# Kernel optimization log

Hardware: AMD Instinct MI355X
Metric: run time of the kernel (lower is better)

Reference implementation:

```python
import jax, jax.numpy as jnp
import numpy as np

N_STATE = 64
N_LAYERS = 4
D_MODEL = 512
D_OUT = 256
BATCH = 16
SEQLEN = 2048


def setup_inputs() -> dict:
    key = jax.random.key(0)
    ks = jax.random.split(key, 16)
    H, N, nl = D_MODEL, N_STATE, N_LAYERS
    inp = {}
    inp["x"] = jax.random.normal(ks[0], (BATCH, SEQLEN, D_MODEL), dtype=jnp.float32)
    # encoder / decoder dense
    inp["enc_w"] = jax.random.normal(ks[1], (D_MODEL, D_MODEL), jnp.float32) / np.sqrt(D_MODEL)
    inp["enc_b"] = jnp.zeros((D_MODEL,), jnp.float32)
    inp["dec_w"] = jax.random.normal(ks[2], (D_MODEL, D_OUT), jnp.float32) / np.sqrt(D_MODEL)
    inp["dec_b"] = jnp.zeros((D_OUT,), jnp.float32)
    # per-layer LayerNorm
    inp["ln_scale"] = jnp.ones((nl, D_MODEL), jnp.float32)
    inp["ln_bias"] = jnp.zeros((nl, D_MODEL), jnp.float32)
    # per-layer S4 DPLR params (stored as real/imag float pairs)
    inp["lambda_re"] = -0.5 * jnp.ones((nl, H, N), jnp.float32)
    inp["lambda_im"] = jnp.broadcast_to(np.pi * jnp.arange(N, dtype=jnp.float32), (nl, H, N))
    inp["p_re"] = jax.random.normal(ks[3], (nl, H, N), jnp.float32) * 0.5
    inp["p_im"] = jax.random.normal(ks[4], (nl, H, N), jnp.float32) * 0.5
    inp["b_re"] = jax.random.normal(ks[5], (nl, H, N), jnp.float32) * 0.5
    inp["b_im"] = jax.random.normal(ks[6], (nl, H, N), jnp.float32) * 0.5
    inp["c_re"] = jax.random.normal(ks[7], (nl, H, N), jnp.float32) * 0.5
    inp["c_im"] = jax.random.normal(ks[8], (nl, H, N), jnp.float32) * 0.5
    inp["log_step"] = jax.random.uniform(ks[9], (nl, H), jnp.float32, minval=np.log(1e-3), maxval=np.log(1e-1))
    inp["d_param"] = jnp.ones((nl, H), jnp.float32)
    # per-layer output Dense
    inp["out_w"] = jax.random.normal(ks[10], (nl, D_MODEL, D_MODEL), jnp.float32) / np.sqrt(D_MODEL)
    inp["out_b"] = jnp.zeros((nl, D_MODEL), jnp.float32)
    return inp


def _layer_norm(x, scale, bias, eps=1e-6):
    mu = jnp.mean(x, axis=-1, keepdims=True)
    var = jnp.mean(jnp.square(x - mu), axis=-1, keepdims=True)
    return (x - mu) * jax.lax.rsqrt(var + eps) * scale + bias


def _kernel_dplr(Lam, P, B, C, step, L):
    # Lam,P,B,C: [H,N] complex64; step: [H] float32 -> K: [H,L] float32
    theta = (2.0 * np.pi / L) * jnp.arange(L, dtype=jnp.float32)
    Omega = jnp.exp(-1j * theta)                        # [L] roots of unity
    g = (2.0 / step)[:, None] * ((1.0 - Omega) / (1.0 + Omega))[None, :]  # [H,L]
    c = 2.0 / (1.0 + Omega)                             # [L]
    r = 1.0 / (g[:, :, None] - Lam[:, None, :])         # [H,L,N] resolvent (Cauchy)
    Cc, Pc = jnp.conj(C), jnp.conj(P)
    k00 = jnp.einsum("hn,hln->hl", Cc * B, r)
    k01 = jnp.einsum("hn,hln->hl", Cc * P, r)
    k10 = jnp.einsum("hn,hln->hl", Pc * B, r)
    k11 = jnp.einsum("hn,hln->hl", Pc * P, r)
    at_roots = c[None, :] * (k00 - k01 * (1.0 / (1.0 + k11)) * k10)  # [H,L]
    return jnp.fft.ifft(at_roots, n=L, axis=-1).real


def _s4_apply(u, Lam, P, B, C, step, D):
    # u: [Bt,L,H]; causal FFT convolution with kernel K[h,:] per channel
    L = u.shape[1]
    K = _kernel_dplr(Lam, P, B, C, step, L)             # [H,L]
    ud = jnp.fft.rfft(u, n=2 * L, axis=1)               # [Bt,L+1,H]
    Kd = jnp.fft.rfft(K, n=2 * L, axis=-1)              # [H,L+1]
    y = jnp.fft.irfft(ud * Kd.T[None], n=2 * L, axis=1)[:, :L]
    return y + D[None, None, :] * u


def reference(x, enc_w, enc_b, ln_scale, ln_bias, lambda_re, lambda_im,
              p_re, p_im, b_re, b_im, c_re, c_im, log_step, d_param,
              out_w, out_b, dec_w, dec_b):
    h = x @ enc_w + enc_b
    n_layers = ln_scale.shape[0]
    for i in range(n_layers):
        skip = h
        z = _layer_norm(h, ln_scale[i], ln_bias[i])
        Lam = lambda_re[i] + 1j * lambda_im[i]
        P = p_re[i] + 1j * p_im[i]
        B = b_re[i] + 1j * b_im[i]
        C = c_re[i] + 1j * c_im[i]
        z = _s4_apply(z, Lam, P, B, C, jnp.exp(log_step[i]), d_param[i])
        z = jax.nn.gelu(z)
        z = z @ out_w[i] + out_b[i]
        h = skip + z  # dropout=0.0 -> identity
    logits = h @ dec_w + dec_b
    return jax.nn.log_softmax(logits, axis=-1)
```

## Files before the change

### kernel.cpp

```cpp
#include <hip/hip_runtime.h>
#include <hip/hip_bf16.h>

#define NLAY 4
#define DH   512
#define NST  64
#define NB   16
#define SL   2048
#define NDO  256
#define BL   (NB*SL)
#define KDIM 512
#define TWOPI 6.283185307179586476925287

typedef unsigned short u16;
typedef __attribute__((ext_vector_type(8))) short  short8v;
typedef __attribute__((ext_vector_type(8))) unsigned short ushort8v;
typedef __attribute__((ext_vector_type(4))) float  f32x4;

#define RCPF(x) __builtin_amdgcn_rcpf(x)

__device__ __forceinline__ float bf2f(u16 v){
  union { unsigned u; float f; } x; x.u = ((unsigned)v) << 16; return x.f;
}
__device__ __forceinline__ u16 f2bf(float f){
  union { float f; unsigned u; } x; x.f = f;
  unsigned u = x.u;
  unsigned r = u + 0x7fffu + ((u >> 16) & 1u);
  return (u16)(r >> 16);
}
__device__ __forceinline__ void cmulw(float& xr, float& xi, float wr, float wi){
  float tr = xr*wr - xi*wi;
  xi = fmaf(xr, wi, xi*wr);
  xr = tr;
}
__device__ __forceinline__ float gelu_fast(float v){
  const float c0 = 0.7978845608028654f;
  float u = c0 * fmaf(0.044715f, v*v*v, v);
  return v * RCPF(1.0f + __expf(-2.0f * u));
}

template<int SGN>
__device__ __forceinline__ void dft4w(float& r0, float& i0, float& r1, float& i1,
                                      float& r2, float& i2, float& r3, float& i3){
  const float t0r = r0 + r2, t0i = i0 + i2;
  const float t1r = r0 - r2, t1i = i0 - i2;
  const float t2r = r1 + r3, t2i = i1 + i3;
  const float t3r = r1 - r3, t3i = i1 - i3;
  r0 = t0r + t2r; i0 = t0i + t2i;
  r2 = t0r - t2r; i2 = t0i - t2i;
  if (SGN < 0){ r1 = t1r + t3i; i1 = t1i - t3r; r3 = t1r - t3i; i3 = t1i + t3r; }
  else        { r1 = t1r - t3i; i1 = t1i + t3r; r3 = t1r + t3i; i3 = t1i - t3r; }
}

template<int SGN>
__device__ __forceinline__ void dft16(float* re, float* im){
#pragma unroll
  for (int b = 0; b < 4; b++)
    dft4w<SGN>(re[b], im[b], re[4+b], im[4+b], re[8+b], im[8+b], re[12+b], im[12+b]);
  const float C1 = 0.92387953251128675613f, S1_ = 0.38268343236508977172f;
  const float C2 = 0.70710678118654752440f;
  const float sg = (SGN < 0) ? -1.f : 1.f;
  cmulw(re[5],  im[5],   C1,  sg*S1_);
  cmulw(re[9],  im[9],   C2,  sg*C2);
  cmulw(re[13], im[13],  S1_, sg*C1);
  cmulw(re[6],  im[6],   C2,  sg*C2);
  cmulw(re[10], im[10],  0.f, sg*1.f);
  cmulw(re[14], im[14], -C2,  sg*C2);
  cmulw(re[7],  im[7],   S1_, sg*C1);
  cmulw(re[11], im[11], -C2,  sg*C2);
  cmulw(re[15], im[15], -C1,  sg*(-S1_));
#pragma unroll
  for (int c = 0; c < 4; c++)
    dft4w<SGN>(re[4*c], im[4*c], re[4*c+1], im[4*c+1], re[4*c+2], im[4*c+2], re[4*c+3], im[4*c+3]);
  float tr_, ti_;
#define SWP(A,B) tr_=re[A]; re[A]=re[B]; re[B]=tr_; ti_=im[A]; im[A]=im[B]; im[B]=ti_;
  SWP(1,4) SWP(2,8) SWP(3,12) SWP(6,9) SWP(7,13) SWP(11,14)
#undef SWP
}

__device__ __forceinline__ int cxpad(int i){ return i + (i >> 4) + ((i >> 8) << 1); }
#define CXSZ 4384

__device__ __forceinline__ void fwd4096(float* re, float* im, float2* cx, int t){
  dft16<-1>(re, im);
  const float a0 = -(float)(TWOPI/4096.0) * (float)t;
#pragma unroll
  for (int k = 0; k < 16; k++){
    if (k){ float sn = __sinf(a0*(float)k), cs = __cosf(a0*(float)k); cmulw(re[k], im[k], cs, sn); }
    cx[cxpad(t + 256*k)] = make_float2(re[k], im[k]);
  }
  __syncthreads();
  const int k1 = t >> 4, m2 = t & 15;
  const int b2 = k1*256 + m2;
#pragma unroll
  for (int j = 0; j < 16; j++){ float2 v = cx[cxpad(b2 + 16*j)]; re[j] = v.x; im[j] = v.y; }
  dft16<-1>(re, im);
  const float b0 = -(float)(TWOPI/256.0) * (float)m2;
#pragma unroll
  for (int k = 0; k < 16; k++){
    if (k){ float sn = __sinf(b0*(float)k), cs = __cosf(b0*(float)k); cmulw(re[k], im[k], cs, sn); }
    cx[cxpad(b2 + 16*k)] = make_float2(re[k], im[k]);
  }
  __syncthreads();
#pragma unroll
  for (int j = 0; j < 16; j++){ float2 v = cx[cxpad(16*t + j)]; re[j] = v.x; im[j] = v.y; }
  dft16<-1>(re, im);
}

__device__ __forceinline__ void inv4096(float* re, float* im, float2* cx, int t){
  dft16<1>(re, im);
#pragma unroll
  for (int j = 0; j < 16; j++) cx[cxpad(16*t + j)] = make_float2(re[j], im[j]);
  __syncthreads();
  const int k1 = t >> 4, m2 = t & 15;
  const int b2 = k1*256 + m2;
  const float b0 = (float)(TWOPI/256.0) * (float)m2;
#pragma unroll
  for (int k = 0; k < 16; k++){
    float2 v = cx[cxpad(b2 + 16*k)];
    re[k] = v.x; im[k] = v.y;
    if (k){ float sn = __sinf(b0*(float)k), cs = __cosf(b0*(float)k); cmulw(re[k], im[k], cs, sn); }
  }
  dft16<1>(re, im);
#pragma unroll
  for (int j = 0; j < 16; j++) cx[cxpad(b2 + 16*j)] = make_float2(re[j], im[j]);
  __syncthreads();
  const float a0 = (float)(TWOPI/4096.0) * (float)t;
#pragma unroll
  for (int k = 0; k < 16; k++){
    float2 v = cx[cxpad(t + 256*k)];
    re[k] = v.x; im[k] = v.y;
    if (k){ float sn = __sinf(a0*(float)k), cs = __cosf(a0*(float)k); cmulw(re[k], im[k], cs, sn); }
  }
  dft16<1>(re, im);
}

__global__ __launch_bounds__(256) void prep_k(
  const float* __restrict__ lam_re, const float* __restrict__ lam_im,
  const float* __restrict__ p_re,  const float* __restrict__ p_im,
  const float* __restrict__ b_re,  const float* __restrict__ b_im,
  const float* __restrict__ c_re,  const float* __restrict__ c_im,
  float4* __restrict__ cwA, float4* __restrict__ cwB, float* __restrict__ cwS)
{
  const int i = blockIdx.x * 256 + threadIdx.x;
  const float lr = lam_re[i], li = lam_im[i];
  const float pr = p_re[i],  pi = p_im[i];
  const float br = b_re[i],  bi = b_im[i];
  const float cr = c_re[i],  ci = c_im[i];
  cwA[i] = make_float4(lr, li, cr*br + ci*bi, cr*bi - ci*br);
  cwB[i] = make_float4(cr*pr + ci*pi, cr*pi - ci*pr, pr*br + pi*bi, pr*bi - pi*br);
  cwS[i] = pr*pr + pi*pi;
}

__global__ __launch_bounds__(256) void cauchy_k(
    const float4* __restrict__ cwA, const float4* __restrict__ cwB,
    const float* __restrict__ cwS, const float* __restrict__ lstep,
    float2* __restrict__ Kd)
{
  const int t = threadIdx.x;
  const int h = blockIdx.y, lay = blockIdx.z;
  const int lb = blockIdx.x * 256 + t;
  const int wb = (lay*DH + h) * NST;
  const float tw0 = 2.0f * expf(-lstep[lay*DH + h]);

  float T[4], gi[4];
#pragma unroll
  for (int j = 0; j < 4; j++){
    float sn, cs;
    sincosf((float)(TWOPI/4096.0) * (float)(lb + 512*j), &sn, &cs);
    T[j] = sn * RCPF(cs);
    gi[j] = tw0 * T[j];
  }

  float k00r[4]={0,0,0,0}, k00i[4]={0,0,0,0};
  float k01r[4]={0,0,0,0}, k01i[4]={0,0,0,0};
  float k10r[4]={0,0,0,0}, k10i[4]={0,0,0,0};
  float k11r[4]={0,0,0,0}, k11i[4]={0,0,0,0};

#pragma unroll 2
  for (int n = 0; n < NST; n++){
    const float4 A  = cwA[wb + n];
    const float4 Bv = cwB[wb + n];
    const float w11 = cwS[wb + n];
    const float nlr = -A.x;
    const float dr2 = A.x * A.x;
#pragma unroll
    for (int j = 0; j < 4; j++){
      const float di = gi[j] - A.y;
      const float sI = RCPF(fmaf(di, di, dr2));
      const float ivr = nlr * sI, ivi = -di * sI;
      k00r[j] = fmaf(A.z,  ivr, fmaf(-A.w,  ivi, k00r[j]));
      k00i[j] = fmaf(A.z,  ivi, fmaf( A.w,  ivr, k00i[j]));
      k01r[j] = fmaf(Bv.x, ivr, fmaf(-Bv.y, ivi, k01r[j]));
      k01i[j] = fmaf(Bv.x, ivi, fmaf( Bv.y, ivr, k01i[j]));
      k10r[j] = fmaf(Bv.z, ivr, fmaf(-Bv.w, ivi, k10r[j]));
      k10i[j] = fmaf(Bv.z, ivi, fmaf( Bv.w, ivr, k10i[j]));
      k11r[j] = fmaf(w11,  ivr, k11r[j]);
      k11i[j] = fmaf(w11,  ivi, k11i[j]);
    }
  }

  float2* kp = Kd + (size_t)(lay*DH + h) * 4096;
#pragma unroll
  for (int j = 0; j < 4; j++){
    const float d1r = 1.f + k11r[j], d1i = k11i[j];
    const float idn = RCPF(fmaf(d1r, d1r, d1i*d1i));
    const float wr = k01r[j]*k10r[j] - k01i[j]*k10i[j];
    const float wi = k01r[j]*k10i[j] + k01i[j]*k10r[j];
    const float vr = fmaf(wr, d1r,  wi*d1i) * idn;
    const float vi = fmaf(wi, d1r, -wr*d1i) * idn;
    const float sr = k00r[j] - vr, si = k00i[j] - vi;
    kp[lb + 512*j] = make_float2(fmaf(-T[j], si, sr), fmaf(T[j], sr, si));
  }
}

__global__ __launch_bounds__(256) void kdfft_k(float2* __restrict__ Kd){
  __shared__ float  ar[SL], ai[SL];
  __shared__ float2 cx[CXSZ];
  const int t = threadIdx.x;
  const size_t base = (size_t)blockIdx.x * 4096;
#pragma unroll
  for (int q = 0; q < 8; q++){
    const int l = t + 256*q;
    float2 v = Kd[base + l];
    const int brv = __brev((unsigned)l) >> 21;
    ar[brv] = v.x; ai[brv] = v.y;
  }
  __syncthreads();

  for (int s = 0; s < 11; s++){
    const int half = 1 << s;
    const float fac = (float)(TWOPI) / (float)(2 << s);
#pragma unroll
    for (int q = 0; q < 4; q++){
      const int v = t + 256*q;
      const int pos = v & (half - 1);
      const int i0 = ((v >> s) << (s+1)) + pos;
      const int i1 = i0 + half;
      const float ang = fac * (float)pos;
      const float wc = __cosf(ang), ws = __sinf(ang);
      const float xr = ar[i1], xi = ai[i1];
      const float tr = wc*xr - ws*xi, ti = fmaf(wc, xi, ws*xr);
      const float ur_ = ar[i0], ui_ = ai[i0];
      ar[i0] = ur_ + tr; ai[i0] = ui_ + ti;
      ar[i1] = ur_ - tr; ai[i1] = ui_ - ti;
    }
    __syncthreads();
  }

  float re[16], im[16];
#pragma unroll
  for (int j = 0; j < 16; j++){
    re[j] = (j < 8) ? ar[t + 256*j] * (1.0f/2048.f) : 0.f;
    im[j] = 0.f;
  }
  fwd4096(re, im, cx, t);
  float2* kp = Kd + base + 16*t;
#pragma unroll
  for (int k = 0; k < 16; k += 2)
    *(float4*)(kp + k) = make_float4(re[k], im[k], re[k+1], im[k+1]);
}

__global__ __launch_bounds__(256) void wconv_k(const float* __restrict__ src,
    u16* __restrict__ dst, int K, int N){
  __shared__ u16 tile[64][72];
  const size_t mb = (size_t)blockIdx.z * K * N;
  const int k0 = blockIdx.x * 64, n0 = blockIdx.y * 64;
  const int r = threadIdx.x >> 2, c4 = (threadIdx.x & 3) * 16;
  const float* s = src + mb + (size_t)(k0 + r) * N + n0 + c4;
  float4 f0 = *(const float4*)s, f1 = *(const float4*)(s+4);
  float4 f2 = *(const float4*)(s+8), f3 = *(const float4*)(s+12);
  tile[c4+0][r]=f2bf(f0.x); tile[c4+1][r]=f2bf(f0.y); tile[c4+2][r]=f2bf(f0.z); tile[c4+3][r]=f2bf(f0.w);
  tile[c4+4][r]=f2bf(f1.x); tile[c4+5][r]=f2bf(f1.y); tile[c4+6][r]=f2bf(f1.z); tile[c4+7][r]=f2bf(f1.w);
  tile[c4+8][r]=f2bf(f2.x); tile[c4+9][r]=f2bf(f2.y); tile[c4+10][r]=f2bf(f2.z); tile[c4+11][r]=f2bf(f2.w);
  tile[c4+12][r]=f2bf(f3.x); tile[c4+13][r]=f2bf(f3.y); tile[c4+14][r]=f2bf(f3.z); tile[c4+15][r]=f2bf(f3.w);
  __syncthreads();
  u16* d = dst + mb + (size_t)(n0 + r) * K + k0 + c4;
  *(ushort8v*)d       = *(const ushort8v*)&tile[r][c4];
  *(ushort8v*)(d + 8) = *(const ushort8v*)&tile[r][c4 + 8];
}

#define LTILE 32
__device__ __forceinline__ int lnswz(int h){ return ((h >> 1) + (h >> 6)) & 3; }

__global__ __launch_bounds__(256) void lnt_k(const float* __restrict__ hsrc,
    const float* __restrict__ gam, const float* __restrict__ bet,
    u16* __restrict__ zT){
  __shared__ u16 tile[DH][LTILE];
  __shared__ float smu[LTILE], srs[LTILE];
  const int t = threadIdx.x;
  const int b = blockIdx.y, l0 = blockIdx.x * LTILE;
  const int r = t >> 3, hb = (t & 7) * 64;
  const float* p = hsrc + ((size_t)b * SL + l0 + r) * DH + hb;
  float s = 0.f, sq = 0.f;
#pragma unroll
  for (int j4 = 0; j4 < 16; j4++){
    float4 v = *(const float4*)(p + j4*4);
    s  += (v.x + v.y) + (v.z + v.w);
    sq += v.x*v.x + v.y*v.y + v.z*v.z + v.w*v.w;
    const int h0 = hb + j4*4;
    tile[h0+0][r ^ (lnswz(h0+0) << 3)] = f2bf(v.x);
    tile[h0+1][r ^ (lnswz(h0+1) << 3)] = f2bf(v.y);
    tile[h0+2][r ^ (lnswz(h0+2) << 3)] = f2bf(v.z);
    tile[h0+3][r ^ (lnswz(h0+3) << 3)] = f2bf(v.w);
  }
  s  += __shfl_xor(s, 1);  sq += __shfl_xor(sq, 1);
  s  += __shfl_xor(s, 2);  sq += __shfl_xor(sq, 2);
  s  += __shfl_xor(s, 4);  sq += __shfl_xor(sq, 4);
  if ((t & 7) == 0){
    const float mu = s * (1.0f/DH);
    smu[r] = mu;
    srs[r] = rsqrtf(sq * (1.0f/DH) - mu*mu + 1e-6f);
  }
  __syncthreads();

#pragma unroll
  for (int hh = 0; hh < 2; hh++){
    const int h = t + hh*256;
    const float g = gam[h], be = bet[h];
    const int sw = lnswz(h);
    u16* dst = zT + ((size_t)b * DH + h) * SL + l0;
#pragma unroll
    for (int og = 0; og < 4; og++){
      const int lg = og ^ sw;
      ushort8v v = *(const ushort8v*)&tile[h][og*8];
      const float4 m0 = *(const float4*)&smu[lg*8];
      const float4 m1 = *(const float4*)&smu[lg*8 + 4];
      const float4 r0 = *(const float4*)&srs[lg*8];
      const float4 r1 = *(const float4*)&srs[lg*8 + 4];
      ushort8v o;
      o[0] = f2bf(fmaf(bf2f((u16)v[0]) - m0.x, r0.x*g, be));
      o[1] = f2bf(fmaf(bf2f((u16)v[1]) - m0.y, r0.y*g, be));
      o[2] = f2bf(fmaf(bf2f((u16)v[2]) - m0.z, r0.z*g, be));
      o[3] = f2bf(fmaf(bf2f((u16)v[3]) - m0.w, r0.w*g, be));
      o[4] = f2bf(fmaf(bf2f((u16)v[4]) - m1.x, r1.x*g, be));
      o[5] = f2bf(fmaf(bf2f((u16)v[5]) - m1.y, r1.y*g, be));
      o[6] = f2bf(fmaf(bf2f((u16)v[6]) - m1.z, r1.z*g, be));
      o[7] = f2bf(fmaf(bf2f((u16)v[7]) - m1.w, r1.w*g, be));
      *(ushort8v*)(dst + lg*8) = o;
    }
  }
}

__global__ __launch_bounds__(256) void s4conv_k(
    const u16* __restrict__ zT, const float2* __restrict__ Kd,
    const float* __restrict__ dpar, u16* __restrict__ yT)
{
  __shared__ float2 cx[CXSZ];
  const int t = threadIdx.x;
  const int wg = blockIdx.x;
  const int h = wg & 511, bp = wg >> 9;
  const u16* r1 = zT + ((size_t)(2*bp) * DH + h) * SL;
  const u16* r2 = r1 + (size_t)DH * SL;
  float ur1[8], ur2[8];
  float re[16], im[16];
#pragma unroll
  for (int j = 0; j < 8; j++){
    ur1[j] = bf2f(r1[t + 256*j]);
    ur2[j] = bf2f(r2[t + 256*j]);
    re[j] = ur1[j]; im[j] = ur2[j];
  }
#pragma unroll
  for (int j = 8; j < 16; j++){ re[j] = 0.f; im[j] = 0.f; }

  fwd4096(re, im, cx, t);

  const float2* kp = Kd + (size_t)h * 4096 + 16*t;
#pragma unroll
  for (int k = 0; k < 16; k += 2){
    float4 w2 = *(const float4*)(kp + k);
    cmulw(re[k],   im[k],   w2.x, w2.y);
    cmulw(re[k+1], im[k+1], w2.z, w2.w);
  }

  inv4096(re, im, cx, t);

  const float Dv = dpar[h];
  u16* y1 = yT + ((size_t)(2*bp) * DH + h) * SL;
  u16* y2 = y1 + (size_t)DH * SL;
#pragma unroll
  for (int j = 0; j < 8; j++){
    float v1 = fmaf(re[j], (1.0f/4096.f), Dv * ur1[j]);
    float v2 = fmaf(im[j], (1.0f/4096.f), Dv * ur2[j]);
    y1[t + 256*j] = f2bf(gelu_fast(v1));
    y2[t + 256*j] = f2bf(gelu_fast(v2));
  }
}

template<int AMODE, bool RESID>
__global__ __launch_bounds__(256) void gemm_k(
    const void* __restrict__ Aptr, const u16* __restrict__ Wt,
    const float* __restrict__ bias,
    const float* __restrict__ resid, float* __restrict__ Cout,
    int Mb, int N)
{
  __shared__ u16 As[128][40];
  __shared__ u16 Bs[128][40];
  const int t = threadIdx.x;
  const int n0 = blockIdx.x * 128, m0 = blockIdx.y * 128, bb = blockIdx.z;
  const int lane = t & 63, wv = t >> 6;
  const int wm = (wv >> 1) * 64, wn = (wv & 1) * 64;
  f32x4 acc[4][4];
#pragma unroll
  for (int mi = 0; mi < 4; mi++)
#pragma unroll
    for (int ni = 0; ni < 4; ni++) acc[mi][ni] = {0.f, 0.f, 0.f, 0.f};

  const u16*  Ab = (const u16*)Aptr;
  const float* Af = (const float*)Aptr;
  const size_t Abase = (AMODE == 1) ? (size_t)bb * KDIM * Mb : 0;

  for (int k0 = 0; k0 < KDIM; k0 += 32){
    __syncthreads();
    if (AMODE == 1){
      const int kk = t >> 3, ch = t & 7;
      const u16* srca = Ab + Abase + (size_t)(k0 + kk) * Mb + m0 + ch*16;
      ushort8v v0 = *(const ushort8v*)srca;
      ushort8v v1 = *(const ushort8v*)(srca + 8);
      const int col = (kk & 7) | (((kk >> 3) ^ (ch & 3)) << 3);
#pragma unroll
      for (int i = 0; i < 8; i++){
        As[ch*16 + i][col]     = (u16)v0[i];
        As[ch*16 + 8 + i][col] = (u16)v1[i];
      }
    } else if (AMODE == 0){
      const int r = t >> 1, kh = (t & 1) << 4;
      const u16* srca = Ab + (size_t)(m0 + r) * KDIM + k0 + kh;
      ushort8v v0 = *(const ushort8v*)srca;
      ushort8v v1 = *(const ushort8v*)(srca + 8);
      const int s3 = (r >> 4) & 3;
      const int c0 = (((kh >> 3) ^ s3) << 3);
      const int c1 = ((((kh >> 3) + 1) ^ s3) << 3);
      *(ushort8v*)&As[r][c0] = v0;
      *(ushort8v*)&As[r][c1] = v1;
    } else {
      const int r = t >> 1, kh = (t & 1) << 4;
      const float* sf = Af + (size_t)(m0 + r) * KDIM + k0 + kh;
      float4 f0 = *(const float4*)sf,     f1 = *(const float4*)(sf + 4);
      float4 f2 = *(const float4*)(sf+8), f3 = *(const float4*)(sf + 12);
      ushort8v v0, v1;
      v0[0]=f2bf(f0.x); v0[1]=f2bf(f0.y); v0[2]=f2bf(f0.z); v0[3]=f2bf(f0.w);
      v0[4]=f2bf(f1.x); v0[5]=f2bf(f1.y); v0[6]=f2bf(f1.z); v0[7]=f2bf(f1.w);
      v1[0]=f2bf(f2.x); v1[1]=f2bf(f2.y); v1[2]=f2bf(f2.z); v1[3]=f2bf(f2.w);
      v1[4]=f2bf(f3.x); v1[5]=f2bf(f3.y); v1[6]=f2bf(f3.z); v1[7]=f2bf(f3.w);
      const int s3 = (r >> 4) & 3;
      const int c0 = (((kh >> 3) ^ s3) << 3);
      const int c1 = ((((kh >> 3) + 1) ^ s3) << 3);
      *(ushort8v*)&As[r][c0] = v0;
      *(ushort8v*)&As[r][c1] = v1;
    }
    {
      const int r = t >> 1, kh = (t & 1) << 4;
      const u16* srcb = Wt + (size_t)(n0 + r) * KDIM + k0 + kh;
      ushort8v v0 = *(const ushort8v*)srcb;
      ushort8v v1 = *(const ushort8v*)(srcb + 8);
      const int s3 = (r >> 4) & 3;
      const int c0 = (((kh >> 3) ^ s3) << 3);
      const int c1 = ((((kh >> 3) + 1) ^ s3) << 3);
      *(ushort8v*)&Bs[r][c0] = v0;
      *(ushort8v*)&Bs[r][c1] = v1;
    }
    __syncthreads();

    const int ko = (lane >> 4) * 8;
    const int fr = lane & 15;
    short8v af[4], bf[4];
#pragma unroll
    for (int mi = 0; mi < 4; mi++){
      const int col = (((ko >> 3) ^ (((wm >> 4) + mi) & 3)) << 3);
      af[mi] = *(const short8v*)&As[wm + mi*16 + fr][col];
    }
#pragma unroll
    for (int ni = 0; ni < 4; ni++){
      const int col = (((ko >> 3) ^ (((wn >> 4) + ni) & 3)) << 3);
      bf[ni] = *(const short8v*)&Bs[wn + ni*16 + fr][col];
    }
#pragma unroll
    for (int mi = 0; mi < 4; mi++)
#pragma unroll
      for (int ni = 0; ni < 4; ni++)
        acc[mi][ni] = __builtin_amdgcn_mfma_f32_16x16x32_bf16(af[mi], bf[ni], acc[mi][ni], 0, 0, 0);
  }

  const int fr = lane & 15;
  const int rq = (lane >> 4) * 4;
#pragma unroll
  for (int mi = 0; mi < 4; mi++){
#pragma unroll
    for (int ni = 0; ni < 4; ni++){
      const int gn = n0 + wn + ni*16 + fr;
      const float bs = bias[gn];
#pragma unroll
      for (int q = 0; q < 4; q++){
        const int gm = m0 + wm + mi*16 + rq + q;
        const size_t idx = ((size_t)bb * Mb + gm) * N + gn;
        float v = acc[mi][ni][q] + bs;
        if (RESID) v += resid[idx];
        Cout[idx] = v;
      }
    }
  }
}

__global__ __launch_bounds__(256) void lsm_k(float* __restrict__ o){
  const int row = blockIdx.x * 4 + (threadIdx.x >> 6);
  const int lane = threadIdx.x & 63;
  float* p = o + (size_t)row * NDO + lane * 4;
  float4 v = *(const float4*)p;
  float mx = fmaxf(fmaxf(v.x, v.y), fmaxf(v.z, v.w));
#pragma unroll
  for (int q = 32; q; q >>= 1) mx = fmaxf(mx, __shfl_xor(mx, q));
  float e = __expf(v.x - mx) + __expf(v.y - mx) + __expf(v.z - mx) + __expf(v.w - mx);
#pragma unroll
  for (int q = 32; q; q >>= 1) e += __shfl_xor(e, q);
  const float lse = mx + __logf(e);
  v.x -= lse; v.y -= lse; v.z -= lse; v.w -= lse;
  *(float4*)p = v;
}

extern "C" void kernel_launch(void* const* d_in, const int* in_sizes, int n_in,
                              void* d_out, int out_size, void* d_ws, size_t ws_size,
                              hipStream_t stream)
{
  (void)in_sizes; (void)n_in; (void)out_size; (void)ws_size;
  const float* x      = (const float*)d_in[0];
  const float* enc_w  = (const float*)d_in[1];
  const float* enc_b  = (const float*)d_in[2];
  const float* dec_w  = (const float*)d_in[3];
  const float* dec_b  = (const float*)d_in[4];
  const float* ln_s   = (const float*)d_in[5];
  const float* ln_b   = (const float*)d_in[6];
  const float* lam_re = (const float*)d_in[7];
  const float* lam_im = (const float*)d_in[8];
  const float* p_re   = (const float*)d_in[9];
  const float* p_im   = (const float*)d_in[10];
  const float* b_re   = (const float*)d_in[11];
  const float* b_im   = (const float*)d_in[12];
  const float* c_re   = (const float*)d_in[13];
  const float* c_im   = (const float*)d_in[14];
  const float* lstep  = (const float*)d_in[15];
  const float* d_par  = (const float*)d_in[16];
  const float* out_w  = (const float*)d_in[17];
  const float* out_b  = (const float*)d_in[18];

  char* ws = (char*)d_ws;
  float*  hbuf = (float*)(ws);
  u16*    zT   = (u16*)  (ws + (size_t)67108864 + 33554432);
  u16*    yT   = (u16*)  (ws + (size_t)67108864 + 2*33554432);
  float2* Kd   = (float2*)(ws + (size_t)67108864 + 3*33554432);
  u16*    Wt   = (u16*)  (ws + (size_t)67108864 + 3*33554432 + 67108864);
  u16*    WtEnc = Wt;
  u16*    WtOut = Wt + 262144;
  u16*    WtDec = Wt + 262144*5;
  float*  outp = (float*)d_out;

  float4* cwA = (float4*)d_out;
  float4* cwB = cwA + 131072;
  float*  cwS = (float*)(cwB + 131072);

  prep_k<<<dim3(NLAY*DH*NST/256), 256, 0, stream>>>(lam_re, lam_im, p_re, p_im,
                                                    b_re, b_im, c_re, c_im, cwA, cwB, cwS);
  wconv_k<<<dim3(8, 8, 1), 256, 0, stream>>>(enc_w, WtEnc, KDIM, DH);
  wconv_k<<<dim3(8, 8, NLAY), 256, 0, stream>>>(out_w, WtOut, KDIM, DH);
  wconv_k<<<dim3(8, 4, 1), 256, 0, stream>>>(dec_w, WtDec, KDIM, NDO);
  cauchy_k<<<dim3(2, DH, NLAY), 256, 0, stream>>>(cwA, cwB, cwS, lstep, Kd);
  kdfft_k<<<dim3(NLAY*DH), 256, 0, stream>>>(Kd);
  gemm_k<2,false><<<dim3(DH/128, BL/128, 1), 256, 0, stream>>>(
      x, WtEnc, enc_b, nullptr, hbuf, BL, DH);
  for (int i = 0; i < NLAY; i++){
    lnt_k<<<dim3(SL/LTILE, NB), 256, 0, stream>>>(hbuf, ln_s + i*DH, ln_b + i*DH, zT);
    s4conv_k<<<dim3((NB/2)*DH), 256, 0, stream>>>(
        zT, Kd + (size_t)i*DH*4096, d_par + i*DH, yT);
    gemm_k<1,true><<<dim3(DH/128, SL/128, NB), 256, 0, stream>>>(
        yT, WtOut + (size_t)i*262144, out_b + i*DH, hbuf, hbuf, SL, DH);
  }
  gemm_k<2,false><<<dim3(NDO/128, BL/128, 1), 256, 0, stream>>>(
      hbuf, WtDec, dec_b, nullptr, outp, BL, NDO);
  lsm_k<<<dim3(BL/4), 256, 0, stream>>>(outp);
}
```

Baseline: 838.2 us.

## Halve FFT shared memory via split real/imag transposes and raise occupancy bounds

The 4096-point FFT transposes now move real and imaginary parts through an LDS buffer of floats, one half at a time with extra barriers, which halves the shared memory per block. s4conv_k stops holding the input in registers and reloads it from global memory at the epilogue, and it gets launch_bounds(256,5). cauchy_k gets launch_bounds(256,4) and its arrays become manually unrolled scalars. Together these aim to fit more blocks per CU, at the cost of twice as many barriers and LDS round trips plus a second global read of the input; f2bf also switches to the library bf16 conversion.

After: 923.6 us. 10.2% more time.

```diff
diff --git a/kernel.cpp b/kernel.cpp
--- a/kernel.cpp
+++ b/kernel.cpp
@@ -22,10 +22,7 @@
   union { unsigned u; float f; } x; x.u = ((unsigned)v) << 16; return x.f;
 }
 __device__ __forceinline__ u16 f2bf(float f){
-  union { float f; unsigned u; } x; x.f = f;
-  unsigned u = x.u;
-  unsigned r = u + 0x7fffu + ((u >> 16) & 1u);
-  return (u16)(r >> 16);
+  union { __hip_bfloat16 h; u16 u; } c; c.h = __float2bfloat16(f); return c.u;
 }
 __device__ __forceinline__ void cmulw(float& xr, float& xi, float wr, float wi){
   float tr = xr*wr - xi*wi;
@@ -80,56 +77,86 @@
 __device__ __forceinline__ int cxpad(int i){ return i + (i >> 4) + ((i >> 8) << 1); }
 #define CXSZ 4384
 
-__device__ __forceinline__ void fwd4096(float* re, float* im, float2* cx, int t){
+__device__ __forceinline__ void fwd4096f(float* re, float* im, float* cxf, int t){
   dft16<-1>(re, im);
   const float a0 = -(float)(TWOPI/4096.0) * (float)t;
 #pragma unroll
-  for (int k = 0; k < 16; k++){
-    if (k){ float sn = __sinf(a0*(float)k), cs = __cosf(a0*(float)k); cmulw(re[k], im[k], cs, sn); }
-    cx[cxpad(t + 256*k)] = make_float2(re[k], im[k]);
-  }
-  __syncthreads();
+  for (int k = 1; k < 16; k++){
+    float sn = __sinf(a0*(float)k), cs = __cosf(a0*(float)k);
+    cmulw(re[k], im[k], cs, sn);
+  }
   const int k1 = t >> 4, m2 = t & 15;
   const int b2 = k1*256 + m2;
 #pragma unroll
-  for (int j = 0; j < 16; j++){ float2 v = cx[cxpad(b2 + 16*j)]; re[j] = v.x; im[j] = v.y; }
+  for (int k = 0; k < 16; k++) cxf[cxpad(t + 256*k)] = re[k];
+  __syncthreads();
+#pragma unroll
+  for (int j = 0; j < 16; j++) re[j] = cxf[cxpad(b2 + 16*j)];
+  __syncthreads();
+#pragma unroll
+  for (int k = 0; k < 16; k++) cxf[cxpad(t + 256*k)] = im[k];
+  __syncthreads();
+#pragma unroll
+  for (int j = 0; j < 16; j++) im[j] = cxf[cxpad(b2 + 16*j)];
   dft16<-1>(re, im);
   const float b0 = -(float)(TWOPI/256.0) * (float)m2;
 #pragma unroll
-  for (int k = 0; k < 16; k++){
-    if (k){ float sn = __sinf(b0*(float)k), cs = __cosf(b0*(float)k); cmulw(re[k], im[k], cs, sn); }
-    cx[cxpad(b2 + 16*k)] = make_float2(re[k], im[k]);
-  }
-  __syncthreads();
-#pragma unroll
-  for (int j = 0; j < 16; j++){ float2 v = cx[cxpad(16*t + j)]; re[j] = v.x; im[j] = v.y; }
+  for (int k = 1; k < 16; k++){
+    float sn = __sinf(b0*(float)k), cs = __cosf(b0*(float)k);
+    cmulw(re[k], im[k], cs, sn);
+  }
+#pragma unroll
+  for (int k = 0; k < 16; k++) cxf[cxpad(b2 + 16*k)] = re[k];
+  __syncthreads();
+#pragma unroll
+  for (int j = 0; j < 16; j++) re[j] = cxf[cxpad(16*t + j)];
+  __syncthreads();
+#pragma unroll
+  for (int k = 0; k < 16; k++) cxf[cxpad(b2 + 16*k)] = im[k];
+  __syncthreads();
+#pragma unroll
+  for (int j = 0; j < 16; j++) im[j] = cxf[cxpad(16*t + j)];
   dft16<-1>(re, im);
 }
 
-__device__ __forceinline__ void inv4096(float* re, float* im, float2* cx, int t){
+__device__ __forceinline__ void inv4096f(float* re, float* im, float* cxf, int t){
   dft16<1>(re, im);
-#pragma unroll
-  for (int j = 0; j < 16; j++) cx[cxpad(16*t + j)] = make_float2(re[j], im[j]);
-  __syncthreads();
   const int k1 = t >> 4, m2 = t & 15;
   const int b2 = k1*256 + m2;
+#pragma unroll
+  for (int j = 0; j < 16; j++) cxf[cxpad(16*t + j)] = re[j];
+  __syncthreads();
+#pragma unroll
+  for (int k = 0; k < 16; k++) re[k] = cxf[cxpad(b2 + 16*k)];
+  __syncthreads();
+#pragma unroll
+  for (int j = 0; j < 16; j++) cxf[cxpad(16*t + j)] = im[j];
+  __syncthreads();
+#pragma unroll
+  for (int k = 0; k < 16; k++) im[k] = cxf[cxpad(b2 + 16*k)];
   const float b0 = (float)(TWOPI/256.0) * (float)m2;
 #pragma unroll
-  for (int k = 0; k < 16; k++){
-    float2 v = cx[cxpad(b2 + 16*k)];
-    re[k] = v.x; im[k] = v.y;
-    if (k){ float sn = __sinf(b0*(float)k), cs = __cosf(b0*(float)k); cmulw(re[k], im[k], cs, sn); }
+  for (int k = 1; k < 16; k++){
+    float sn = __sinf(b0*(float)k), cs = __cosf(b0*(float)k);
+    cmulw(re[k], im[k], cs, sn);
   }
   dft16<1>(re, im);
 #pragma unroll
-  for (int j = 0; j < 16; j++) cx[cxpad(b2 + 16*j)] = make_float2(re[j], im[j]);
-  __syncthreads();
+  for (int j = 0; j < 16; j++) cxf[cxpad(b2 + 16*j)] = re[j];
+  __syncthreads();
+#pragma unroll
+  for (int k = 0; k < 16; k++) re[k] = cxf[cxpad(t + 256*k)];
+  __syncthreads();
+#pragma unroll
+  for (int j = 0; j < 16; j++) cxf[cxpad(b2 + 16*j)] = im[j];
+  __syncthreads();
+#pragma unroll
+  for (int k = 0; k < 16; k++) im[k] = cxf[cxpad(t + 256*k)];
   const float a0 = (float)(TWOPI/4096.0) * (float)t;
 #pragma unroll
-  for (int k = 0; k < 16; k++){
-    float2 v = cx[cxpad(t + 256*k)];
-    re[k] = v.x; im[k] = v.y;
-    if (k){ float sn = __sinf(a0*(float)k), cs = __cosf(a0*(float)k); cmulw(re[k], im[k], cs, sn); }
+  for (int k = 1; k < 16; k++){
+    float sn = __sinf(a0*(float)k), cs = __cosf(a0*(float)k);
+    cmulw(re[k], im[k], cs, sn);
   }
   dft16<1>(re, im);
 }
@@ -151,7 +178,7 @@
   cwS[i] = pr*pr + pi*pi;
 }
 
-__global__ __launch_bounds__(256) void cauchy_k(
+__global__ __launch_bounds__(256, 4) void cauchy_k(
     const float4* __restrict__ cwA, const float4* __restrict__ cwB,
     const float* __restrict__ cwS, const float* __restrict__ lstep,
     float2* __restrict__ Kd)
@@ -162,60 +189,58 @@
   const int wb = (lay*DH + h) * NST;
   const float tw0 = 2.0f * expf(-lstep[lay*DH + h]);
 
-  float T[4], gi[4];
-#pragma unroll
-  for (int j = 0; j < 4; j++){
-    float sn, cs;
-    sincosf((float)(TWOPI/4096.0) * (float)(lb + 512*j), &sn, &cs);
-    T[j] = sn * RCPF(cs);
-    gi[j] = tw0 * T[j];
-  }
-
-  float k00r[4]={0,0,0,0}, k00i[4]={0,0,0,0};
-  float k01r[4]={0,0,0,0}, k01i[4]={0,0,0,0};
-  float k10r[4]={0,0,0,0}, k10i[4]={0,0,0,0};
-  float k11r[4]={0,0,0,0}, k11i[4]={0,0,0,0};
-
-#pragma unroll 2
+  float T0,T1,T2,T3, g0,g1,g2,g3;
+  { float sn, cs;
+    sincosf((float)(TWOPI/4096.0)*(float)(lb       ), &sn, &cs); T0 = sn*RCPF(cs); g0 = tw0*T0;
+    sincosf((float)(TWOPI/4096.0)*(float)(lb +  512), &sn, &cs); T1 = sn*RCPF(cs); g1 = tw0*T1;
+    sincosf((float)(TWOPI/4096.0)*(float)(lb + 1024), &sn, &cs); T2 = sn*RCPF(cs); g2 = tw0*T2;
+    sincosf((float)(TWOPI/4096.0)*(float)(lb + 1536), &sn, &cs); T3 = sn*RCPF(cs); g3 = tw0*T3;
+  }
+
+  float k00r0=0,k00i0=0,k01r0=0,k01i0=0,k10r0=0,k10i0=0,k11r0=0,k11i0=0;
+  float k00r1=0,k00i1=0,k01r1=0,k01i1=0,k10r1=0,k10i1=0,k11r1=0,k11i1=0;
+  float k00r2=0,k00i2=0,k01r2=0,k01i2=0,k10r2=0,k10i2=0,k11r2=0,k11i2=0;
+  float k00r3=0,k00i3=0,k01r3=0,k01i3=0,k10r3=0,k10i3=0,k11r3=0,k11i3=0;
+
   for (int n = 0; n < NST; n++){
     const float4 A  = cwA[wb + n];
     const float4 Bv = cwB[wb + n];
     const float w11 = cwS[wb + n];
     const float nlr = -A.x;
     const float dr2 = A.x * A.x;
-#pragma unroll
-    for (int j = 0; j < 4; j++){
-      const float di = gi[j] - A.y;
-      const float sI = RCPF(fmaf(di, di, dr2));
-      const float ivr = nlr * sI, ivi = -di * sI;
-      k00r[j] = fmaf(A.z,  ivr, fmaf(-A.w,  ivi, k00r[j]));
-      k00i[j] = fmaf(A.z,  ivi, fmaf( A.w,  ivr, k00i[j]));
-      k01r[j] = fmaf(Bv.x, ivr, fmaf(-Bv.y, ivi, k01r[j]));
-      k01i[j] = fmaf(Bv.x, ivi, fmaf( Bv.y, ivr, k01i[j]));
-      k10r[j] = fmaf(Bv.z, ivr, fmaf(-Bv.w, ivi, k10r[j]));
-      k10i[j] = fmaf(Bv.z, ivi, fmaf( Bv.w, ivr, k10i[j]));
-      k11r[j] = fmaf(w11,  ivr, k11r[j]);
-      k11i[j] = fmaf(w11,  ivi, k11i[j]);
-    }
+#define CSTEP(J) { \
+    const float di = g##J - A.y; \
+    const float sI = RCPF(fmaf(di, di, dr2)); \
+    const float ivr = nlr * sI, ivi = -di * sI; \
+    k00r##J = fmaf(A.z,  ivr, fmaf(-A.w,  ivi, k00r##J)); \
+    k00i##J = fmaf(A.z,  ivi, fmaf( A.w,  ivr, k00i##J)); \
+    k01r##J = fmaf(Bv.x, ivr, fmaf(-Bv.y, ivi, k01r##J)); \
+    k01i##J = fmaf(Bv.x, ivi, fmaf( Bv.y, ivr, k01i##J)); \
+    k10r##J = fmaf(Bv.z, ivr, fmaf(-Bv.w, ivi, k10r##J)); \
+    k10i##J = fmaf(Bv.z, ivi, fmaf( Bv.w, ivr, k10i##J)); \
+    k11r##J = fmaf(w11,  ivr, k11r##J); \
+    k11i##J = fmaf(w11,  ivi, k11i##J); }
+    CSTEP(0) CSTEP(1) CSTEP(2) CSTEP(3)
+#undef CSTEP
   }
 
   float2* kp = Kd + (size_t)(lay*DH + h) * 4096;
-#pragma unroll
-  for (int j = 0; j < 4; j++){
-    const float d1r = 1.f + k11r[j], d1i = k11i[j];
-    const float idn = RCPF(fmaf(d1r, d1r, d1i*d1i));
-    const float wr = k01r[j]*k10r[j] - k01i[j]*k10i[j];
-    const float wi = k01r[j]*k10i[j] + k01i[j]*k10r[j];
-    const float vr = fmaf(wr, d1r,  wi*d1i) * idn;
-    const float vi = fmaf(wi, d1r, -wr*d1i) * idn;
-    const float sr = k00r[j] - vr, si = k00i[j] - vi;
-    kp[lb + 512*j] = make_float2(fmaf(-T[j], si, sr), fmaf(T[j], sr, si));
-  }
+#define COUT(J, LOFF) { \
+    const float d1r = 1.f + k11r##J, d1i = k11i##J; \
+    const float idn = RCPF(fmaf(d1r, d1r, d1i*d1i)); \
+    const float wr = k01r##J*k10r##J - k01i##J*k10i##J; \
+    const float wi = k01r##J*k10i##J + k01i##J*k10r##J; \
+    const float vr = fmaf(wr, d1r,  wi*d1i) * idn; \
+    const float vi = fmaf(wi, d1r, -wr*d1i) * idn; \
+    const float sr = k00r##J - vr, si = k00i##J - vi; \
+    kp[lb + LOFF] = make_float2(fmaf(-T##J, si, sr), fmaf(T##J, sr, si)); }
+  COUT(0, 0) COUT(1, 512) COUT(2, 1024) COUT(3, 1536)
+#undef COUT
 }
 
 __global__ __launch_bounds__(256) void kdfft_k(float2* __restrict__ Kd){
-  __shared__ float  ar[SL], ai[SL];
-  __shared__ float2 cx[CXSZ];
+  __shared__ float ar[SL], ai[SL];
+  __shared__ float cxf[CXSZ];
   const int t = threadIdx.x;
   const size_t base = (size_t)blockIdx.x * 4096;
 #pragma unroll
@@ -253,7 +278,7 @@
     re[j] = (j < 8) ? ar[t + 256*j] * (1.0f/2048.f) : 0.f;
     im[j] = 0.f;
   }
-  fwd4096(re, im, cx, t);
+  fwd4096f(re, im, cxf, t);
   float2* kp = Kd + base + 16*t;
 #pragma unroll
   for (int k = 0; k < 16; k += 2)
@@ -341,28 +366,26 @@
   }
 }
 
-__global__ __launch_bounds__(256) void s4conv_k(
+__global__ __launch_bounds__(256, 5) void s4conv_k(
     const u16* __restrict__ zT, const float2* __restrict__ Kd,
     const float* __restrict__ dpar, u16* __restrict__ yT)
 {
-  __shared__ float2 cx[CXSZ];
+  __shared__ float cxf[CXSZ];
   const int t = threadIdx.x;
   const int wg = blockIdx.x;
   const int h = wg & 511, bp = wg >> 9;
   const u16* r1 = zT + ((size_t)(2*bp) * DH + h) * SL;
   const u16* r2 = r1 + (size_t)DH * SL;
-  float ur1[8], ur2[8];
   float re[16], im[16];
 #pragma unroll
   for (int j = 0; j < 8; j++){
-    ur1[j] = bf2f(r1[t + 256*j]);
-    ur2[j] = bf2f(r2[t + 256*j]);
-    re[j] = ur1[j]; im[j] = ur2[j];
+    re[j] = bf2f(r1[t + 256*j]);
+    im[j] = bf2f(r2[t + 256*j]);
   }
 #pragma unroll
   for (int j = 8; j < 16; j++){ re[j] = 0.f; im[j] = 0.f; }
 
-  fwd4096(re, im, cx, t);
+  fwd4096f(re, im, cxf, t);
 
   const float2* kp = Kd + (size_t)h * 4096 + 16*t;
 #pragma unroll
@@ -372,15 +395,17 @@
     cmulw(re[k+1], im[k+1], w2.z, w2.w);
   }
 
-  inv4096(re, im, cx, t);
+  inv4096f(re, im, cxf, t);
 
   const float Dv = dpar[h];
   u16* y1 = yT + ((size_t)(2*bp) * DH + h) * SL;
   u16* y2 = y1 + (size_t)DH * SL;
 #pragma unroll
   for (int j = 0; j < 8; j++){
-    float v1 = fmaf(re[j], (1.0f/4096.f), Dv * ur1[j]);
-    float v2 = fmaf(im[j], (1.0f/4096.f), Dv * ur2[j]);
+    const float u1 = bf2f(r1[t + 256*j]);
+    const float u2 = bf2f(r2[t + 256*j]);
+    float v1 = fmaf(re[j], (1.0f/4096.f), Dv * u1);
+    float v2 = fmaf(im[j], (1.0f/4096.f), Dv * u2);
     y1[t + 256*j] = f2bf(gelu_fast(v1));
     y2[t + 256*j] = f2bf(gelu_fast(v2));
   }
```
